# Kernel tuning notes

Hardware: AMD Instinct MI355X
Metric: run time of the kernel (lower is better)

The kernel has to match this reference:

```python
import jax, jax.numpy as jnp
import numpy as np

N = 8192      # total nodes
B = 64        # graphs in batch
NPG = 128     # nodes per graph (equal-size graphs; idx sorted)
D_IN = 256
H = 256       # hidden_dim (d_model)
NH = 4        # nhead
HD = H // NH
FF = 2 * H    # dim_feedforward
NC = 16       # n_class


def setup_inputs() -> dict:
    key = jax.random.key(0)
    ks = jax.random.split(key, 16)
    def rn(k, shp, scale=0.05):
        return jax.random.normal(k, shp, jnp.float32) * scale
    inp = {}
    inp["x_in"] = jax.random.normal(ks[0], (N, D_IN), jnp.float32)
    # scale adjacency so each row sums ~1 to keep activations well-conditioned
    inp["adj"] = jax.random.uniform(ks[1], (N, N), jnp.float32) * (2.0 / N)
    inp["idx"] = jnp.repeat(jnp.arange(B, dtype=jnp.int32), NPG)
    inp["cum_nodes"] = jnp.full((B,), NPG, jnp.int32)
    # fc1
    inp["W1"] = rn(ks[2], (D_IN, H)); inp["b1"] = jnp.zeros((H,), jnp.float32)
    # transformer encoder layer (eval mode, dropout inactive)
    inp["in_w"] = rn(ks[3], (H, 3 * H)); inp["in_b"] = jnp.zeros((3 * H,), jnp.float32)
    inp["out_w"] = rn(ks[4], (H, H));    inp["out_b"] = jnp.zeros((H,), jnp.float32)
    inp["ln1_s"] = jnp.ones((H,), jnp.float32); inp["ln1_b"] = jnp.zeros((H,), jnp.float32)
    inp["ff1_w"] = rn(ks[5], (H, FF)); inp["ff1_b"] = jnp.zeros((FF,), jnp.float32)
    inp["ff2_w"] = rn(ks[6], (FF, H)); inp["ff2_b"] = jnp.zeros((H,), jnp.float32)
    inp["ln2_s"] = jnp.ones((H,), jnp.float32); inp["ln2_b"] = jnp.zeros((H,), jnp.float32)
    # fc3 / fc4
    inp["W3"] = rn(ks[7], (H, H));  inp["b3"] = jnp.zeros((H,), jnp.float32)
    inp["W4"] = rn(ks[8], (H, NC)); inp["b4"] = jnp.zeros((NC,), jnp.float32)
    return inp


def _layer_norm(x, s, b):
    mu = x.mean(-1, keepdims=True)
    xc = x - mu
    return xc * jax.lax.rsqrt((xc * xc).mean(-1, keepdims=True) + 1e-5) * s + b


def reference(x_in, adj, idx, cum_nodes, W1, b1, in_w, in_b, out_w, out_b,
              ln1_s, ln1_b, ff1_w, ff1_b, ff2_w, ff2_b, ln2_s, ln2_b,
              W3, b3, W4, b4):
    Bg = cum_nodes.shape[0]
    n = x_in.shape[0] // Bg  # equal-size graphs -> pad_sequence == reshape
    x = x_in @ W1 + b1                      # fc1
    x = jax.nn.relu(adj @ x)                # adjacency message passing
    p = x.reshape(Bg, n, H)                 # pack: idx is sorted, graphs equal size
    # --- TransformerEncoderLayer (post-LN, relu FFN, eval mode) ---
    qkv = p @ in_w + in_b                   # [B, n, 3H]
    q, k, v = jnp.split(qkv, 3, axis=-1)
    q = q.reshape(Bg, n, NH, HD); k = k.reshape(Bg, n, NH, HD); v = v.reshape(Bg, n, NH, HD)
    att = jax.nn.softmax(jnp.einsum('bqhd,bkhd->bhqk', q, k) / np.sqrt(HD), axis=-1)
    o = jnp.einsum('bhqk,bkhd->bqhd', att, v).reshape(Bg, n, H) @ out_w + out_b
    y = _layer_norm(p + o, ln1_s, ln1_b)
    ff = jax.nn.relu(y @ ff1_w + ff1_b) @ ff2_w + ff2_b
    y = _layer_norm(y + ff, ln2_s, ln2_b)
    # --- unpack + scatter-add pooling over graphs ---
    flat = y.reshape(Bg * n, H)
    pooled = jax.ops.segment_sum(flat, idx, num_segments=Bg)  # [B, H]
    out = jax.nn.relu(pooled @ W3 + b3) @ W4 + b4
    return jax.nn.log_softmax(out, axis=-1)
```

## Files before the change

kernel.cpp:

```cpp
#include <hip/hip_runtime.h>

typedef float fx4 __attribute__((ext_vector_type(4)));
typedef short s16x8 __attribute__((ext_vector_type(8)));
typedef short s16x4 __attribute__((ext_vector_type(4)));
typedef unsigned short ushort_t;

__device__ __forceinline__ short f2bf(float f) {
  union { float f; unsigned u; } v; v.f = f;
  unsigned r = v.u + 0x7FFFu + ((v.u >> 16) & 1u);
  return (short)(r >> 16);
}

__device__ __forceinline__ float bf2f(short h) {
  union { float f; unsigned u; } v;
  v.u = ((unsigned)(unsigned short)h) << 16;
  return v.f;
}

__device__ __forceinline__ unsigned cvt_pk_bf16(float a, float b) {
  unsigned r;
  asm("v_cvt_pk_bf16_f32 %0, %1, %2" : "=v"(r) : "v"(a), "v"(b));
  return r;
}

__device__ __forceinline__ s16x8 cvt8(fx4 a, fx4 b) {
  union { s16x8 s; unsigned u[4]; } w;
  w.u[0] = cvt_pk_bf16(a[0], a[1]);
  w.u[1] = cvt_pk_bf16(a[2], a[3]);
  w.u[2] = cvt_pk_bf16(b[0], b[1]);
  w.u[3] = cvt_pk_bf16(b[2], b[3]);
  return w.s;
}

__device__ __forceinline__ void gload16(const void* g, void* l) {
  __builtin_amdgcn_global_load_lds(
      (const __attribute__((address_space(1))) unsigned int*)g,
      (__attribute__((address_space(3))) unsigned int*)l, 16, 0, 0);
}

__global__ __launch_bounds__(256) void prep_kernel(
    const float* __restrict__ W1, const float* __restrict__ in_w,
    const float* __restrict__ out_w, const float* __restrict__ ff1_w,
    const float* __restrict__ ff2_w,
    ushort_t* __restrict__ W1t, ushort_t* __restrict__ in_wT,
    ushort_t* __restrict__ out_wT, ushort_t* __restrict__ ff1t,
    ushort_t* __restrict__ ff2t) {
  const int bid = blockIdx.x, t = threadIdx.x;
  const float* W; ushort_t* Wt; int K, N, base;
  if (bid < 256)       { W = W1;    Wt = W1t;    K = 256; N = 256; base = 0; }
  else if (bid < 1024) { W = in_w;  Wt = in_wT;  K = 256; N = 768; base = 256; }
  else if (bid < 1280) { W = out_w; Wt = out_wT; K = 256; N = 256; base = 1024; }
  else if (bid < 1792) { W = ff1_w; Wt = ff1t;   K = 256; N = 512; base = 1280; }
  else                 { W = ff2_w; Wt = ff2t;   K = 512; N = 256; base = 1792; }
  const int idx = (bid - base) * 256 + t;
  const int k = idx / N, n = idx - k * N;
  Wt[(size_t)n * K + k] = (ushort_t)f2bf(W[idx]);
}

template<int MF, bool AF32, int OUTM, bool RELU, bool RES>
__global__ __launch_bounds__(256) void gemm2(
    const void* __restrict__ Av, const ushort_t* __restrict__ Bt,
    const float* __restrict__ bias, const float* __restrict__ res,
    const float* __restrict__ lns, const float* __restrict__ lnb,
    float* __restrict__ Cf, ushort_t* __restrict__ Cb,
    int M, int N, int K, int kLen) {
  constexpr int BM = MF * 16;
  __shared__ __align__(16) ushort_t Asm[2][BM * 64];
  __shared__ __align__(16) ushort_t Bsm[256 * 64];
  const int t = threadIdx.x, lane = t & 63, wave = t >> 6;
  const int bm = blockIdx.y * BM;
  const int bn = (OUTM == 5) ? 0 : blockIdx.x * 256;
  const int kOff = (OUTM == 5) ? blockIdx.x * kLen : 0;
  const int wn = wave * 64, fr = lane & 15, fq = lane >> 4;
  const int NT = kLen >> 6;
  const int x0 = ((fq) ^ (fr & 7)) * 8;
  const int x1 = ((4 + fq) ^ (fr & 7)) * 8;
  fx4 acc[MF][4] = {};

  const int gl = lane >> 3, gc = lane & 7;
  const int gsw = (gc ^ gl) * 8;
  const ushort_t* Bgl =
      Bt + (size_t)(bn + wave * 64 + gl) * K + kOff + gsw;
  const ushort_t* Agl =
      (const ushort_t*)Av + (size_t)(bm + wave * (BM / 4) + gl) * K + kOff + gsw;
  constexpr int TPR = 256 / BM;
  const int arow = t / TPR;
  const int ac0 = (t % TPR) * (BM / 4);
  const float* Afp = (const float*)Av + (size_t)(bm + arow) * K + kOff + ac0;
  fx4 R[MF / 2][2];

  auto issueB = [&](int kt) {
    #pragma unroll
    for (int i = 0; i < 8; ++i)
      gload16(Bgl + (size_t)i * 8 * K + kt * 64, &Bsm[wave * 4096 + i * 512]);
  };
  auto issueAg = [&](int buf, int kt) {
    #pragma unroll
    for (int i = 0; i < MF / 2; ++i)
      gload16(Agl + (size_t)i * 8 * K + kt * 64,
              &Asm[buf][wave * (BM * 16) + i * 512]);
  };
  auto loadR = [&](int kt) {
    #pragma unroll
    for (int w = 0; w < MF / 2; ++w) {
      R[w][0] = *(const fx4*)(Afp + kt * 64 + w * 8);
      R[w][1] = *(const fx4*)(Afp + kt * 64 + w * 8 + 4);
    }
  };
  auto writeA = [&](int buf) {
    #pragma unroll
    for (int w = 0; w < MF / 2; ++w) {
      const int cs = ((ac0 >> 3) + w) ^ (arow & 7);
      *(s16x8*)&Asm[buf][arow * 64 + cs * 8] = cvt8(R[w][0], R[w][1]);
    }
  };

  if constexpr (AF32) { loadR(0); issueB(0); writeA(0); loadR(1); }
  else { issueAg(0, 0); issueB(0); }
  __syncthreads();

  #pragma unroll 1
  for (int kt = 0; kt < NT; ++kt) {
    const int cur = kt & 1;
    s16x8 b0[4], b1[4], a0[MF], a1[MF];
    #pragma unroll
    for (int nf = 0; nf < 4; ++nf) {
      b0[nf] = *(const s16x8*)&Bsm[(wn + nf * 16 + fr) * 64 + x0];
      b1[nf] = *(const s16x8*)&Bsm[(wn + nf * 16 + fr) * 64 + x1];
    }
    #pragma unroll
    for (int mf = 0; mf < MF; ++mf)
      a0[mf] = *(const s16x8*)&Asm[cur][(mf * 16 + fr) * 64 + x0];
    asm volatile("s_waitcnt lgkmcnt(0)" ::: "memory");
    if (kt + 1 < NT) {
      if constexpr (AF32) {
        writeA(cur ^ 1);
        if (kt + 2 < NT) loadR(kt + 2);
        issueB(kt + 1);
      } else {
        issueAg(cur ^ 1, kt + 1);
        issueB(kt + 1);
      }
    }
    #pragma unroll
    for (int mf = 0; mf < MF; ++mf)
      #pragma unroll
      for (int nf = 0; nf < 4; ++nf)
        acc[mf][nf] = __builtin_amdgcn_mfma_f32_16x16x32_bf16(
            a0[mf], b0[nf], acc[mf][nf], 0, 0, 0);
    #pragma unroll
    for (int mf = 0; mf < MF; ++mf)
      a1[mf] = *(const s16x8*)&Asm[cur][(mf * 16 + fr) * 64 + x1];
    #pragma unroll
    for (int mf = 0; mf < MF; ++mf)
      #pragma unroll
      for (int nf = 0; nf < 4; ++nf)
        acc[mf][nf] = __builtin_amdgcn_mfma_f32_16x16x32_bf16(
            a1[mf], b1[nf], acc[mf][nf], 0, 0, 0);
    __syncthreads();
  }

  if constexpr (OUTM == 3) {
    #pragma unroll
    for (int mf = 0; mf < MF; ++mf)
      #pragma unroll
      for (int nf = 0; nf < 4; ++nf) {
        const int col = bn + wn + nf * 16 + fr;
        const float bb = bias[col];
        s16x4 w;
        #pragma unroll
        for (int r = 0; r < 4; ++r) w[r] = f2bf(acc[mf][nf][r] + bb);
        *(s16x4*)&Cb[(size_t)col * M + bm + mf * 16 + fq * 4] = w;
      }
  } else if constexpr (OUTM == 5) {
    ushort_t* po = Cb + (size_t)blockIdx.x * ((size_t)M * 256);
    #pragma unroll
    for (int mf = 0; mf < MF; ++mf)
      #pragma unroll
      for (int nf = 0; nf < 4; ++nf)
        #pragma unroll
        for (int r = 0; r < 4; ++r)
          po[(size_t)(bm + mf * 16 + fq * 4 + r) * 256 + wn + nf * 16 + fr] =
              (ushort_t)f2bf(acc[mf][nf][r]);
  } else {
    #pragma unroll
    for (int mf = 0; mf < MF; ++mf)
      #pragma unroll
      for (int nf = 0; nf < 4; ++nf) {
        const int col = bn + wn + nf * 16 + fr;
        const float bb = bias[col];
        #pragma unroll
        for (int r = 0; r < 4; ++r) {
          const int row = bm + mf * 16 + fq * 4 + r;
          float x = acc[mf][nf][r] + bb;
          if constexpr (RES) x += res[(size_t)row * N + col];
          if constexpr (RELU) x = fmaxf(x, 0.f);
          if constexpr (OUTM == 0 || OUTM == 2) Cf[(size_t)row * N + col] = x;
          if constexpr (OUTM == 1 || OUTM == 2)
            Cb[(size_t)row * N + col] = (ushort_t)f2bf(x);
        }
      }
  }
}

__global__ __launch_bounds__(256) void relu_reduce8(
    const ushort_t* __restrict__ part, float* __restrict__ p,
    ushort_t* __restrict__ pb) {
  const size_t i = ((size_t)blockIdx.x * 256 + threadIdx.x) * 8;
  const size_t S = 8192ull * 256ull;
  float a[8] = {};
  #pragma unroll
  for (int j = 0; j < 8; ++j) {
    const s16x8 v = *(const s16x8*)(part + j * S + i);
    #pragma unroll
    for (int c = 0; c < 8; ++c) a[c] += bf2f(v[c]);
  }
  fx4 v0, v1;
  #pragma unroll
  for (int c = 0; c < 4; ++c) {
    v0[c] = fmaxf(a[c], 0.f);
    v1[c] = fmaxf(a[c + 4], 0.f);
  }
  *(fx4*)(p + i) = v0;
  *(fx4*)(p + i + 4) = v1;
  s16x8 w;
  #pragma unroll
  for (int c = 0; c < 4; ++c) { w[c] = f2bf(v0[c]); w[c + 4] = f2bf(v1[c]); }
  *(s16x8*)(pb + i) = w;
}

__global__ __launch_bounds__(256) void att_fused(
    const ushort_t* __restrict__ qkv, ushort_t* __restrict__ attout) {
  __shared__ float k_s[128][68];
  __shared__ float v_s[128][68];
  __shared__ float s_s[128][129];
  __shared__ float pm[2][128];
  __shared__ float ps[2][128];
  const int bh = blockIdx.x, b = bh >> 2, h = bh & 3;
  const int t = threadIdx.x;
  const ushort_t* qb = qkv + (size_t)b * 128 * 768 + h * 64;
  for (int u = t; u < 1024; u += 256) {
    const int n = u >> 3, d8 = (u & 7) * 8;
    const s16x8 kk = *(const s16x8*)(qb + (size_t)n * 768 + 256 + d8);
    const s16x8 vv = *(const s16x8*)(qb + (size_t)n * 768 + 512 + d8);
    #pragma unroll
    for (int c = 0; c < 8; ++c) {
      k_s[n][d8 + c] = bf2f(kk[c]);
      v_s[n][d8 + c] = bf2f(vv[c]);
    }
  }
  const int row = t & 127, kh = t >> 7;
  fx4 qr[16];
  {
    const s16x8* q8 = (const s16x8*)(qb + (size_t)row * 768);
    #pragma unroll
    for (int j = 0; j < 8; ++j) {
      const s16x8 qv = q8[j];
      qr[2*j][0] = bf2f(qv[0]); qr[2*j][1] = bf2f(qv[1]);
      qr[2*j][2] = bf2f(qv[2]); qr[2*j][3] = bf2f(qv[3]);
      qr[2*j+1][0] = bf2f(qv[4]); qr[2*j+1][1] = bf2f(qv[5]);
      qr[2*j+1][2] = bf2f(qv[6]); qr[2*j+1][3] = bf2f(qv[7]);
    }
  }
  __syncthreads();
  float m = -1e30f;
  for (int j = 0; j < 64; ++j) {
    const int jj = kh * 64 + j;
    const fx4* kr = (const fx4*)&k_s[jj][0];
    float s0 = 0.f, s1 = 0.f, s2 = 0.f, s3 = 0.f;
    #pragma unroll
    for (int c = 0; c < 16; c += 4) {
      fx4 k0 = kr[c], k1 = kr[c + 1], k2 = kr[c + 2], k3 = kr[c + 3];
      s0 += qr[c][0]*k0[0] + qr[c][1]*k0[1] + qr[c][2]*k0[2] + qr[c][3]*k0[3];
      s1 += qr[c+1][0]*k1[0] + qr[c+1][1]*k1[1] + qr[c+1][2]*k1[2] + qr[c+1][3]*k1[3];
      s2 += qr[c+2][0]*k2[0] + qr[c+2][1]*k2[1] + qr[c+2][2]*k2[2] + qr[c+2][3]*k2[3];
      s3 += qr[c+3][0]*k3[0] + qr[c+3][1]*k3[1] + qr[c+3][2]*k3[2] + qr[c+3][3]*k3[3];
    }
    const float s = (s0 + s1 + s2 + s3) * 0.125f;
    s_s[row][jj] = s;
    m = fmaxf(m, s);
  }
  pm[kh][row] = m;
  __syncthreads();
  const float m2 = fmaxf(pm[0][row], pm[1][row]);
  float sum = 0.f;
  for (int j = 0; j < 64; ++j) {
    const int jj = kh * 64 + j;
    const float e = __expf(s_s[row][jj] - m2);
    s_s[row][jj] = e;
    sum += e;
  }
  ps[kh][row] = sum;
  __syncthreads();
  const int row2 = t >> 1, dh = (t & 1) * 32;
  const float inv = 1.f / (ps[0][row2] + ps[1][row2]);
  fx4 acc4[8] = {};
  for (int k = 0; k < 128; ++k) {
    const float e = s_s[row2][k];
    const fx4* vr = (const fx4*)&v_s[k][dh];
    #pragma unroll
    for (int c = 0; c < 8; ++c) acc4[c] += e * vr[c];
  }
  ushort_t* orow = attout + (size_t)(b * 128 + row2) * 256 + h * 64 + dh;
  #pragma unroll
  for (int c = 0; c < 8; ++c) {
    const fx4 v = acc4[c] * inv;
    s16x4 w;
    #pragma unroll
    for (int j = 0; j < 4; ++j) w[j] = f2bf(v[j]);
    *(s16x4*)(orow + c * 4) = w;
  }
}

__global__ __launch_bounds__(256) void tail_kernel(
    const ushort_t* __restrict__ attout, const ushort_t* __restrict__ out_wT,
    const float* __restrict__ out_b, const float* __restrict__ p_res,
    const float* __restrict__ ln1_s, const float* __restrict__ ln1_b,
    const ushort_t* __restrict__ ff1t, const float* __restrict__ ff1_b,
    const ushort_t* __restrict__ ff2t, const float* __restrict__ ff2_b,
    const float* __restrict__ ln2_s, const float* __restrict__ ln2_b,
    float* __restrict__ pooled4) {
  __shared__ __align__(16) ushort_t Asm[2][32 * 64];
  __shared__ __align__(16) ushort_t Bsm[256 * 64];
  __shared__ __align__(16) ushort_t y_s[32 * 256];
  __shared__ __align__(16) ushort_t f1_s[32 * 512];
  __shared__ float red_s[128], red_q[128];
  const int t = threadIdx.x, lane = t & 63, wave = t >> 6;
  const int bq = blockIdx.x, bm = bq * 32;
  const int wn = wave * 64, fr = lane & 15, fq = lane >> 4;
  const int x0 = (fq ^ (fr & 7)) * 8, x1 = ((4 + fq) ^ (fr & 7)) * 8;
  const int gl = lane >> 3, gc = lane & 7, gsw = (gc ^ gl) * 8;

  fx4 acc[2][4] = {};
  {
    const ushort_t* Agl = attout + (size_t)(bm + wave * 8 + gl) * 256 + gsw;
    const ushort_t* Bgl = out_wT + (size_t)(wave * 64 + gl) * 256 + gsw;
    auto issueA = [&](int buf, int kt) {
      gload16(Agl + kt * 64, &Asm[buf][wave * 512]);
    };
    auto issueB = [&](int kt) {
      #pragma unroll
      for (int i = 0; i < 8; ++i)
        gload16(Bgl + (size_t)i * 8 * 256 + kt * 64,
                &Bsm[wave * 4096 + i * 512]);
    };
    issueA(0, 0); issueB(0);
    __syncthreads();
    #pragma unroll 1
    for (int kt = 0; kt < 4; ++kt) {
      const int cur = kt & 1;
      s16x8 b0[4], b1[4], a0[2], a1[2];
      #pragma unroll
      for (int nf = 0; nf < 4; ++nf) {
        b0[nf] = *(const s16x8*)&Bsm[(wn + nf * 16 + fr) * 64 + x0];
        b1[nf] = *(const s16x8*)&Bsm[(wn + nf * 16 + fr) * 64 + x1];
      }
      #pragma unroll
      for (int mf = 0; mf < 2; ++mf) {
        a0[mf] = *(const s16x8*)&Asm[cur][(mf * 16 + fr) * 64 + x0];
        a1[mf] = *(const s16x8*)&Asm[cur][(mf * 16 + fr) * 64 + x1];
      }
      asm volatile("s_waitcnt lgkmcnt(0)" ::: "memory");
      if (kt < 3) { issueA(cur ^ 1, kt + 1); issueB(kt + 1); }
      #pragma unroll
      for (int mf = 0; mf < 2; ++mf)
        #pragma unroll
        for (int nf = 0; nf < 4; ++nf) {
          acc[mf][nf] = __builtin_amdgcn_mfma_f32_16x16x32_bf16(
              a0[mf], b0[nf], acc[mf][nf], 0, 0, 0);
          acc[mf][nf] = __builtin_amdgcn_mfma_f32_16x16x32_bf16(
              a1[mf], b1[nf], acc[mf][nf], 0, 0, 0);
        }
      __syncthreads();
    }
  }
  float yv[2][4][4];
  #pragma unroll
  for (int mf = 0; mf < 2; ++mf)
    #pragma unroll
    for (int nf = 0; nf < 4; ++nf) {
      const int col = wn + nf * 16 + fr;
      #pragma unroll
      for (int r = 0; r < 4; ++r) {
        const int row = bm + mf * 16 + fq * 4 + r;
        yv[mf][nf][r] = acc[mf][nf][r] + out_b[col] +
                        p_res[(size_t)row * 256 + col];
      }
    }
  {
    #pragma unroll
    for (int mf = 0; mf < 2; ++mf)
      #pragma unroll
      for (int r = 0; r < 4; ++r) {
        float s = yv[mf][0][r] + yv[mf][1][r] + yv[mf][2][r] + yv[mf][3][r];
        float q = yv[mf][0][r]*yv[mf][0][r] + yv[mf][1][r]*yv[mf][1][r] +
                  yv[mf][2][r]*yv[mf][2][r] + yv[mf][3][r]*yv[mf][3][r];
        #pragma unroll
        for (int off = 1; off < 16; off <<= 1) {
          s += __shfl_xor(s, off, 64);
          q += __shfl_xor(q, off, 64);
        }
        if (fr == 0) {
          red_s[(mf * 16 + fq * 4 + r) * 4 + wave] = s;
          red_q[(mf * 16 + fq * 4 + r) * 4 + wave] = q;
        }
      }
    __syncthreads();
    #pragma unroll
    for (int mf = 0; mf < 2; ++mf)
      #pragma unroll
      for (int r = 0; r < 4; ++r) {
        const int rl = mf * 16 + fq * 4 + r;
        const float st = red_s[rl*4] + red_s[rl*4+1] + red_s[rl*4+2] + red_s[rl*4+3];
        const float qt = red_q[rl*4] + red_q[rl*4+1] + red_q[rl*4+2] + red_q[rl*4+3];
        const float mu = st * (1.f / 256.f);
        const float rr = rsqrtf(qt * (1.f / 256.f) - mu * mu + 1e-5f);
        #pragma unroll
        for (int nf = 0; nf < 4; ++nf) {
          const int col = wn + nf * 16 + fr;
          const float o = (yv[mf][nf][r] - mu) * rr * ln1_s[col] + ln1_b[col];
          yv[mf][nf][r] = o;
          y_s[rl * 256 + ((col >> 3) ^ (rl & 7)) * 8 + (col & 7)] =
              (ushort_t)f2bf(o);
        }
      }
  }
  __syncthreads();

  #pragma unroll 1
  for (int ng = 0; ng < 2; ++ng) {
    const ushort_t* Bgl = ff1t + (size_t)(ng * 256 + wave * 64 + gl) * 256 + gsw;
    auto issueB = [&](int kt) {
      #pragma unroll
      for (int i = 0; i < 8; ++i)
        gload16(Bgl + (size_t)i * 8 * 256 + kt * 64,
                &Bsm[wave * 4096 + i * 512]);
    };
    fx4 a2[2][4] = {};
    issueB(0);
    #pragma unroll 1
    for (int kt = 0; kt < 4; ++kt) {
      asm volatile("s_waitcnt vmcnt(0)" ::: "memory");
      s16x8 b0[4], b1[4], a0[2], a1[2];
      #pragma unroll
      for (int nf = 0; nf < 4; ++nf) {
        b0[nf] = *(const s16x8*)&Bsm[(wn + nf * 16 + fr) * 64 + x0];
        b1[nf] = *(const s16x8*)&Bsm[(wn + nf * 16 + fr) * 64 + x1];
      }
      #pragma unroll
      for (int mf = 0; mf < 2; ++mf) {
        const int row = mf * 16 + fr;
        a0[mf] = *(const s16x8*)&y_s[row * 256 + ((kt*8 + fq) ^ (row & 7)) * 8];
        a1[mf] = *(const s16x8*)&y_s[row * 256 + ((kt*8 + 4 + fq) ^ (row & 7)) * 8];
      }
      asm volatile("s_waitcnt lgkmcnt(0)" ::: "memory");
      if (kt < 3) issueB(kt + 1);
      #pragma unroll
      for (int mf = 0; mf < 2; ++mf)
        #pragma unroll
        for (int nf = 0; nf < 4; ++nf) {
          a2[mf][nf] = __builtin_amdgcn_mfma_f32_16x16x32_bf16(
              a0[mf], b0[nf], a2[mf][nf], 0, 0, 0);
          a2[mf][nf] = __builtin_amdgcn_mfma_f32_16x16x32_bf16(
              a1[mf], b1[nf], a2[mf][nf], 0, 0, 0);
        }
    }
    #pragma unroll
    for (int mf = 0; mf < 2; ++mf)
      #pragma unroll
      for (int nf = 0; nf < 4; ++nf) {
        const int col = ng * 256 + wn + nf * 16 + fr;
        const float bb = ff1_b[col];
        #pragma unroll
        for (int r = 0; r < 4; ++r) {
          const int rl = mf * 16 + fq * 4 + r;
          const float x = fmaxf(a2[mf][nf][r] + bb, 0.f);
          f1_s[rl * 512 + ((col >> 3) ^ (rl & 7)) * 8 + (col & 7)] =
              (ushort_t)f2bf(x);
        }
      }
  }
  __syncthreads();

  {
    const ushort_t* Bgl = ff2t + (size_t)(wave * 64 + gl) * 512 + gsw;
    auto issueB = [&](int kt) {
      #pragma unroll
      for (int i = 0; i < 8; ++i)
        gload16(Bgl + (size_t)i * 8 * 512 + kt * 64,
                &Bsm[wave * 4096 + i * 512]);
    };
    fx4 a3[2][4] = {};
    issueB(0);
    #pragma unroll 1
    for (int kt = 0; kt < 8; ++kt) {
      asm volatile("s_waitcnt vmcnt(0)" ::: "memory");
      s16x8 b0[4], b1[4], a0[2], a1[2];
      #pragma unroll
      for (int nf = 0; nf < 4; ++nf) {
        b0[nf] = *(const s16x8*)&Bsm[(wn + nf * 16 + fr) * 64 + x0];
        b1[nf] = *(const s16x8*)&Bsm[(wn + nf * 16 + fr) * 64 + x1];
      }
      #pragma unroll
      for (int mf = 0; mf < 2; ++mf) {
        const int row = mf * 16 + fr;
        a0[mf] = *(const s16x8*)&f1_s[row * 512 + ((kt*8 + fq) ^ (row & 7)) * 8];
        a1[mf] = *(const s16x8*)&f1_s[row * 512 + ((kt*8 + 4 + fq) ^ (row & 7)) * 8];
      }
      asm volatile("s_waitcnt lgkmcnt(0)" ::: "memory");
      if (kt < 7) issueB(kt + 1);
      #pragma unroll
      for (int mf = 0; mf < 2; ++mf)
        #pragma unroll
        for (int nf = 0; nf < 4; ++nf) {
          a3[mf][nf] = __builtin_amdgcn_mfma_f32_16x16x32_bf16(
              a0[mf], b0[nf], a3[mf][nf], 0, 0, 0);
          a3[mf][nf] = __builtin_amdgcn_mfma_f32_16x16x32_bf16(
              a1[mf], b1[nf], a3[mf][nf], 0, 0, 0);
        }
    }
    float vv[2][4][4];
    #pragma unroll
    for (int mf = 0; mf < 2; ++mf)
      #pragma unroll
      for (int nf = 0; nf < 4; ++nf) {
        const int col = wn + nf * 16 + fr;
        const float bb = ff2_b[col];
        #pragma unroll
        for (int r = 0; r < 4; ++r)
          vv[mf][nf][r] = a3[mf][nf][r] + bb + yv[mf][nf][r];
      }
    __syncthreads();
    #pragma unroll
    for (int mf = 0; mf < 2; ++mf)
      #pragma unroll
      for (int r = 0; r < 4; ++r) {
        float s = vv[mf][0][r] + vv[mf][1][r] + vv[mf][2][r] + vv[mf][3][r];
        float q = vv[mf][0][r]*vv[mf][0][r] + vv[mf][1][r]*vv[mf][1][r] +
                  vv[mf][2][r]*vv[mf][2][r] + vv[mf][3][r]*vv[mf][3][r];
        #pragma unroll
        for (int off = 1; off < 16; off <<= 1) {
          s += __shfl_xor(s, off, 64);
          q += __shfl_xor(q, off, 64);
        }
        if (fr == 0) {
          red_s[(mf * 16 + fq * 4 + r) * 4 + wave] = s;
          red_q[(mf * 16 + fq * 4 + r) * 4 + wave] = q;
        }
      }
    __syncthreads();
    float colsum[4] = {};
    #pragma unroll
    for (int mf = 0; mf < 2; ++mf)
      #pragma unroll
      for (int r = 0; r < 4; ++r) {
        const int rl = mf * 16 + fq * 4 + r;
        const float st = red_s[rl*4] + red_s[rl*4+1] + red_s[rl*4+2] + red_s[rl*4+3];
        const float qt = red_q[rl*4] + red_q[rl*4+1] + red_q[rl*4+2] + red_q[rl*4+3];
        const float mu = st * (1.f / 256.f);
        const float rr = rsqrtf(qt * (1.f / 256.f) - mu * mu + 1e-5f);
        #pragma unroll
        for (int nf = 0; nf < 4; ++nf) {
          const int col = wn + nf * 16 + fr;
          colsum[nf] += (vv[mf][nf][r] - mu) * rr * ln2_s[col] + ln2_b[col];
        }
      }
    #pragma unroll
    for (int nf = 0; nf < 4; ++nf) {
      colsum[nf] += __shfl_xor(colsum[nf], 16, 64);
      colsum[nf] += __shfl_xor(colsum[nf], 32, 64);
    }
    if (lane < 16)
      #pragma unroll
      for (int nf = 0; nf < 4; ++nf)
        pooled4[(size_t)bq * 256 + wn + nf * 16 + fr] = colsum[nf];
  }
}

__global__ __launch_bounds__(256) void head_kernel(
    const float* __restrict__ pooled4, const float* __restrict__ W3,
    const float* __restrict__ b3, const float* __restrict__ W4,
    const float* __restrict__ b4, float* __restrict__ out) {
  __shared__ float sp[256];
  __shared__ float t1[256];
  __shared__ float logits[16];
  const int b = blockIdx.x, h = threadIdx.x;
  sp[h] = pooled4[(size_t)(b * 4 + 0) * 256 + h] +
          pooled4[(size_t)(b * 4 + 1) * 256 + h] +
          pooled4[(size_t)(b * 4 + 2) * 256 + h] +
          pooled4[(size_t)(b * 4 + 3) * 256 + h];
  __syncthreads();
  float a = b3[h];
  for (int k = 0; k < 256; ++k) a += sp[k] * W3[k * 256 + h];
  t1[h] = fmaxf(a, 0.f);
  __syncthreads();
  if (h < 16) {
    float o = b4[h];
    for (int j = 0; j < 256; ++j) o += t1[j] * W4[j * 16 + h];
    logits[h] = o;
  }
  __syncthreads();
  if (h < 16) {
    float mm = -1e30f;
    #pragma unroll
    for (int c = 0; c < 16; ++c) mm = fmaxf(mm, logits[c]);
    float se = 0.f;
    #pragma unroll
    for (int c = 0; c < 16; ++c) se += __expf(logits[c] - mm);
    out[b * 16 + h] = logits[h] - mm - logf(se);
  }
}

extern "C" void kernel_launch(void* const* d_in, const int* in_sizes, int n_in,
                              void* d_out, int out_size, void* d_ws, size_t ws_size,
                              hipStream_t stream) {
  const float* x_in  = (const float*)d_in[0];
  const float* adj   = (const float*)d_in[1];
  const float* W1    = (const float*)d_in[4];
  const float* b1    = (const float*)d_in[5];
  const float* in_w  = (const float*)d_in[6];
  const float* in_b  = (const float*)d_in[7];
  const float* out_w = (const float*)d_in[8];
  const float* out_b = (const float*)d_in[9];
  const float* ln1_s = (const float*)d_in[10];
  const float* ln1_b = (const float*)d_in[11];
  const float* ff1_w = (const float*)d_in[12];
  const float* ff1_b = (const float*)d_in[13];
  const float* ff2_w = (const float*)d_in[14];
  const float* ff2_b = (const float*)d_in[15];
  const float* ln2_s = (const float*)d_in[16];
  const float* ln2_b = (const float*)d_in[17];
  const float* W3    = (const float*)d_in[18];
  const float* b3    = (const float*)d_in[19];
  const float* W4    = (const float*)d_in[20];
  const float* b4    = (const float*)d_in[21];
  char* ws = (char*)d_ws;
  const size_t MB = 1ull << 20;
  ushort_t* xT      = (ushort_t*)(ws);
  ushort_t* W1t     = (ushort_t*)(ws + 4 * MB);
  ushort_t* in_wT   = (ushort_t*)(ws + 4 * MB + 131072);
  ushort_t* out_wT  = (ushort_t*)(ws + 4 * MB + 524288);
  ushort_t* ff1t    = (ushort_t*)(ws + 4 * MB + 655360);
  ushort_t* ff2t    = (ushort_t*)(ws + 4 * MB + 917504);
  float*    p       = (float*)(ws + 8 * MB);
  ushort_t* p_bf    = (ushort_t*)(ws + 16 * MB);
  ushort_t* qkv_bf  = (ushort_t*)(ws + 20 * MB);
  ushort_t* attout  = (ushort_t*)(ws + 32 * MB);
  float*    pooled4 = (float*)(ws + 36 * MB);
  ushort_t* part    = (ushort_t*)(ws + 37 * MB);
  float*    outp    = (float*)d_out;
  (void)in_sizes; (void)n_in; (void)out_size; (void)ws_size;

  prep_kernel<<<2304, 256, 0, stream>>>(W1, in_w, out_w, ff1_w, ff2_w,
                                        W1t, in_wT, out_wT, ff1t, ff2t);
  gemm2<2, true, 3, false, false><<<dim3(1, 256), 256, 0, stream>>>(
      x_in, W1t, b1, nullptr, nullptr, nullptr, nullptr, xT,
      8192, 256, 256, 256);
  gemm2<4, true, 5, false, false><<<dim3(8, 128), 256, 0, stream>>>(
      adj, xT, nullptr, nullptr, nullptr, nullptr, nullptr, part,
      8192, 256, 8192, 1024);
  relu_reduce8<<<1024, 256, 0, stream>>>(part, p, p_bf);
  gemm2<4, false, 1, false, false><<<dim3(3, 128), 256, 0, stream>>>(
      p_bf, in_wT, in_b, nullptr, nullptr, nullptr, nullptr, qkv_bf,
      8192, 768, 256, 256);
  att_fused<<<256, 256, 0, stream>>>(qkv_bf, attout);
  tail_kernel<<<256, 256, 0, stream>>>(
      attout, out_wT, out_b, p, ln1_s, ln1_b, ff1t, ff1_b,
      ff2t, ff2_b, ln2_s, ln2_b, pooled4);
  head_kernel<<<64, 256, 0, stream>>>(pooled4, W3, b3, W4, b4, outp);
}
```

Baseline: 194.8 us.

## Add dedicated double-buffered adj GEMM kernel with 4-way split-K

Replaces the generic gemm2 split-K path for the adjacency matmul with a specialized kernel that double-buffers both the converted fp32 adj tile and the bf16 xT tile in LDS, using explicit waitcnt/barrier scheduling. Split-K is reduced from 8 to 4 slices (2048 K each), which halves the partial-sum traffic written and reread by the reduction kernel. Fewer blocks (512 vs 1024) lowers parallelism on a large-CU GPU, and the larger LDS footprint may reduce occupancy.

New measurement: 183.3 us. 5.9% less time.

```diff
diff --git a/kernel.cpp b/kernel.cpp
--- a/kernel.cpp
+++ b/kernel.cpp
@@ -69,8 +69,7 @@
   __shared__ __align__(16) ushort_t Bsm[256 * 64];
   const int t = threadIdx.x, lane = t & 63, wave = t >> 6;
   const int bm = blockIdx.y * BM;
-  const int bn = (OUTM == 5) ? 0 : blockIdx.x * 256;
-  const int kOff = (OUTM == 5) ? blockIdx.x * kLen : 0;
+  const int bn = blockIdx.x * 256;
   const int wn = wave * 64, fr = lane & 15, fq = lane >> 4;
   const int NT = kLen >> 6;
   const int x0 = ((fq) ^ (fr & 7)) * 8;
@@ -79,14 +78,13 @@
 
   const int gl = lane >> 3, gc = lane & 7;
   const int gsw = (gc ^ gl) * 8;
-  const ushort_t* Bgl =
-      Bt + (size_t)(bn + wave * 64 + gl) * K + kOff + gsw;
+  const ushort_t* Bgl = Bt + (size_t)(bn + wave * 64 + gl) * K + gsw;
   const ushort_t* Agl =
-      (const ushort_t*)Av + (size_t)(bm + wave * (BM / 4) + gl) * K + kOff + gsw;
+      (const ushort_t*)Av + (size_t)(bm + wave * (BM / 4) + gl) * K + gsw;
   constexpr int TPR = 256 / BM;
   const int arow = t / TPR;
   const int ac0 = (t % TPR) * (BM / 4);
-  const float* Afp = (const float*)Av + (size_t)(bm + arow) * K + kOff + ac0;
+  const float* Afp = (const float*)Av + (size_t)(bm + arow) * K + ac0;
   fx4 R[MF / 2][2];
 
   auto issueB = [&](int kt) {
@@ -172,16 +170,6 @@
         for (int r = 0; r < 4; ++r) w[r] = f2bf(acc[mf][nf][r] + bb);
         *(s16x4*)&Cb[(size_t)col * M + bm + mf * 16 + fq * 4] = w;
       }
-  } else if constexpr (OUTM == 5) {
-    ushort_t* po = Cb + (size_t)blockIdx.x * ((size_t)M * 256);
-    #pragma unroll
-    for (int mf = 0; mf < MF; ++mf)
-      #pragma unroll
-      for (int nf = 0; nf < 4; ++nf)
-        #pragma unroll
-        for (int r = 0; r < 4; ++r)
-          po[(size_t)(bm + mf * 16 + fq * 4 + r) * 256 + wn + nf * 16 + fr] =
-              (ushort_t)f2bf(acc[mf][nf][r]);
   } else {
     #pragma unroll
     for (int mf = 0; mf < MF; ++mf)
@@ -203,14 +191,118 @@
   }
 }
 
-__global__ __launch_bounds__(256) void relu_reduce8(
+__global__ __launch_bounds__(256) void adjmm2(
+    const float* __restrict__ adj, const ushort_t* __restrict__ xT,
+    ushort_t* __restrict__ part) {
+  constexpr int NT = 32;
+  __shared__ __align__(16) ushort_t Asm[2][64 * 64];
+  __shared__ __align__(16) ushort_t Bsm[2][256 * 64];
+  const int t = threadIdx.x, lane = t & 63, wave = t >> 6;
+  const int kh = blockIdx.x, bm = blockIdx.y * 64;
+  const int kOff = kh * 2048;
+  const int wn = wave * 64, fr = lane & 15, fq = lane >> 4;
+  const int x0 = (fq ^ (fr & 7)) * 8, x1 = ((4 + fq) ^ (fr & 7)) * 8;
+  const int gl = lane >> 3, gc = lane & 7, gsw = (gc ^ gl) * 8;
+
+  const ushort_t* Bgl = xT + (size_t)(wn + gl) * 8192 + kOff + gsw;
+  const int arow = t >> 2;
+  const int ac0 = (t & 3) * 16;
+  const float* Afp = adj + (size_t)(bm + arow) * 8192 + kOff + ac0;
+
+  fx4 R[2][2];
+  auto loadR = [&](int kt) {
+    #pragma unroll
+    for (int w = 0; w < 2; ++w) {
+      R[w][0] = *(const fx4*)(Afp + kt * 64 + w * 8);
+      R[w][1] = *(const fx4*)(Afp + kt * 64 + w * 8 + 4);
+    }
+  };
+  auto writeA = [&](int buf) {
+    #pragma unroll
+    for (int w = 0; w < 2; ++w) {
+      const int cs = ((ac0 >> 3) + w) ^ (arow & 7);
+      *(s16x8*)&Asm[buf][arow * 64 + cs * 8] = cvt8(R[w][0], R[w][1]);
+    }
+  };
+  auto issueB = [&](int buf, int kt) {
+    #pragma unroll
+    for (int i = 0; i < 8; ++i)
+      gload16(Bgl + (size_t)i * 8 * 8192 + kt * 64,
+              &Bsm[buf][wave * 4096 + i * 512]);
+  };
+
+  fx4 acc[4][4] = {};
+  loadR(0);
+  issueB(0, 0);
+  writeA(0);
+  loadR(1);
+  asm volatile("s_waitcnt lgkmcnt(0)" ::: "memory");
+  asm volatile("s_waitcnt vmcnt(4)" ::: "memory");
+  __builtin_amdgcn_sched_barrier(0);
+  __builtin_amdgcn_s_barrier();
+  __builtin_amdgcn_sched_barrier(0);
+  issueB(1, 1);
+
+  #pragma unroll 1
+  for (int kt = 0; kt < NT; ++kt) {
+    const int cur = kt & 1;
+    s16x8 a0[4], a1[4], b0[4], b1[4];
+    #pragma unroll
+    for (int mf = 0; mf < 4; ++mf) {
+      a0[mf] = *(const s16x8*)&Asm[cur][(mf * 16 + fr) * 64 + x0];
+      a1[mf] = *(const s16x8*)&Asm[cur][(mf * 16 + fr) * 64 + x1];
+    }
+    #pragma unroll
+    for (int nf = 0; nf < 4; ++nf) {
+      b0[nf] = *(const s16x8*)&Bsm[cur][(wn + nf * 16 + fr) * 64 + x0];
+      b1[nf] = *(const s16x8*)&Bsm[cur][(wn + nf * 16 + fr) * 64 + x1];
+    }
+    if (kt + 1 < NT) {
+      writeA(cur ^ 1);
+      if (kt + 2 < NT) loadR(kt + 2);
+    }
+    #pragma unroll
+    for (int mf = 0; mf < 4; ++mf)
+      #pragma unroll
+      for (int nf = 0; nf < 4; ++nf)
+        acc[mf][nf] = __builtin_amdgcn_mfma_f32_16x16x32_bf16(
+            a0[mf], b0[nf], acc[mf][nf], 0, 0, 0);
+    #pragma unroll
+    for (int mf = 0; mf < 4; ++mf)
+      #pragma unroll
+      for (int nf = 0; nf < 4; ++nf)
+        acc[mf][nf] = __builtin_amdgcn_mfma_f32_16x16x32_bf16(
+            a1[mf], b1[nf], acc[mf][nf], 0, 0, 0);
+    asm volatile("s_waitcnt lgkmcnt(0)" ::: "memory");
+    if (kt + 2 < NT)
+      asm volatile("s_waitcnt vmcnt(4)" ::: "memory");
+    else
+      asm volatile("s_waitcnt vmcnt(0)" ::: "memory");
+    __builtin_amdgcn_sched_barrier(0);
+    __builtin_amdgcn_s_barrier();
+    __builtin_amdgcn_sched_barrier(0);
+    if (kt + 2 < NT) issueB(cur, kt + 2);
+  }
+
+  ushort_t* po = part + (size_t)kh * (8192ull * 256ull);
+  #pragma unroll
+  for (int mf = 0; mf < 4; ++mf)
+    #pragma unroll
+    for (int nf = 0; nf < 4; ++nf)
+      #pragma unroll
+      for (int r = 0; r < 4; ++r)
+        po[(size_t)(bm + mf * 16 + fq * 4 + r) * 256 + wn + nf * 16 + fr] =
+            (ushort_t)f2bf(acc[mf][nf][r]);
+}
+
+__global__ __launch_bounds__(256) void relu_reduce4(
     const ushort_t* __restrict__ part, float* __restrict__ p,
     ushort_t* __restrict__ pb) {
   const size_t i = ((size_t)blockIdx.x * 256 + threadIdx.x) * 8;
   const size_t S = 8192ull * 256ull;
   float a[8] = {};
   #pragma unroll
-  for (int j = 0; j < 8; ++j) {
+  for (int j = 0; j < 4; ++j) {
     const s16x8 v = *(const s16x8*)(part + j * S + i);
     #pragma unroll
     for (int c = 0; c < 8; ++c) a[c] += bf2f(v[c]);
@@ -656,10 +748,8 @@
   gemm2<2, true, 3, false, false><<<dim3(1, 256), 256, 0, stream>>>(
       x_in, W1t, b1, nullptr, nullptr, nullptr, nullptr, xT,
       8192, 256, 256, 256);
-  gemm2<4, true, 5, false, false><<<dim3(8, 128), 256, 0, stream>>>(
-      adj, xT, nullptr, nullptr, nullptr, nullptr, nullptr, part,
-      8192, 256, 8192, 1024);
-  relu_reduce8<<<1024, 256, 0, stream>>>(part, p, p_bf);
+  adjmm2<<<dim3(4, 128), 256, 0, stream>>>(adj, xT, part);
+  relu_reduce4<<<1024, 256, 0, stream>>>(part, p, p_bf);
   gemm2<4, false, 1, false, false><<<dim3(3, 128), 256, 0, stream>>>(
       p_bf, in_wT, in_b, nullptr, nullptr, nullptr, nullptr, qkv_bf,
       8192, 768, 256, 256);
```
